# Kernel tuning notes

Hardware: AMD Instinct MI355X
Metric: run time of the kernel (lower is better)

## Reference

```python
import jax, jax.numpy as jnp
import numpy as np
import math

HIDDEN = 2048
NUM_HEADS = 32
NUM_KV_HEADS = 8
HEAD_DIM = HIDDEN // NUM_HEADS
GROUPS = NUM_HEADS // NUM_KV_HEADS
B, S = 2, 2048


def setup_inputs() -> dict:
    key = jax.random.key(0)
    ks = jax.random.split(key, 9)
    sc = 1.0 / math.sqrt(HIDDEN)
    x = jax.random.normal(ks[0], (B, S, HIDDEN), dtype=jnp.float32)
    # causal mask: 1 where attention allowed, 0 where masked
    mask = jnp.tril(jnp.ones((S, S), dtype=jnp.int32))[None, None, :, :]
    Wq = jax.random.normal(ks[1], (HIDDEN, HIDDEN), dtype=jnp.float32) * sc
    bq = jnp.zeros((HIDDEN,), dtype=jnp.float32)
    Wk = jax.random.normal(ks[2], (NUM_KV_HEADS * HEAD_DIM, HIDDEN), dtype=jnp.float32) * sc
    bk = jnp.zeros((NUM_KV_HEADS * HEAD_DIM,), dtype=jnp.float32)
    Wv = jax.random.normal(ks[3], (NUM_KV_HEADS * HEAD_DIM, HIDDEN), dtype=jnp.float32) * sc
    bv = jnp.zeros((NUM_KV_HEADS * HEAD_DIM,), dtype=jnp.float32)
    Wo = jax.random.normal(ks[4], (HIDDEN, HIDDEN), dtype=jnp.float32) * sc
    bo = jnp.zeros((HIDDEN,), dtype=jnp.float32)
    return {"x": x, "mask": mask, "Wq": Wq, "bq": bq, "Wk": Wk, "bk": bk,
            "Wv": Wv, "bv": bv, "Wo": Wo, "bo": bo}


def reference(x, mask, Wq, bq, Wk, bk, Wv, bv, Wo, bo):
    b, s, _ = x.shape
    # projections (torch Linear: y = x @ W.T + b)
    Q = (x @ Wq.T + bq).reshape(b, s, NUM_HEADS, HEAD_DIM).transpose(0, 2, 1, 3)  # b h s d
    K = (x @ Wk.T + bk).reshape(b, s, NUM_KV_HEADS, HEAD_DIM).transpose(0, 2, 1, 3)
    V = (x @ Wv.T + bv).reshape(b, s, NUM_KV_HEADS, HEAD_DIM).transpose(0, 2, 1, 3)
    # repeat_kv expansion
    K = jnp.repeat(K, GROUPS, axis=1)  # b h s d
    V = jnp.repeat(V, GROUPS, axis=1)
    scores = jnp.einsum('bhqd,bhkd->bhqk', Q, K) / math.sqrt(HEAD_DIM)
    scores = jnp.where(mask == 0, jnp.float32(-jnp.inf), scores)
    w = jax.nn.softmax(scores, axis=-1)
    # dropout is identity in eval mode
    out = jnp.einsum('bhqk,bhkd->bhqd', w, V)
    out = out.transpose(0, 2, 1, 3).reshape(b, s, HIDDEN)
    return out @ Wo.T + bo
```

## Files before the change

kernel.cpp:

```cpp
#include <hip/hip_runtime.h>
#include <hip/hip_bf16.h>
#include <stdint.h>

#define HID   2048
#define SLEN  2048
#define NB    2
#define NHEADS 32
#define NKVH   8
#define HDIM   64
#define KVW    512

typedef __bf16 bf16_t;
typedef __bf16 bf16x2 __attribute__((ext_vector_type(2)));
typedef __bf16 bf16x4 __attribute__((ext_vector_type(4)));
typedef __bf16 bf16x8 __attribute__((ext_vector_type(8)));
typedef float  f32x4  __attribute__((ext_vector_type(4)));

__device__ __forceinline__ f32x4 mfma16(bf16x8 a, bf16x8 b, f32x4 c) {
  return __builtin_amdgcn_mfma_f32_16x16x32_bf16(a, b, c, 0, 0, 0);
}

__device__ __forceinline__ void gl2lds16(const bf16_t* g, bf16_t* l) {
  __builtin_amdgcn_global_load_lds(
      (const __attribute__((address_space(1))) void*)g,
      (__attribute__((address_space(3))) void*)l,
      16, 0, 0);
}

__device__ __forceinline__ float fast_exp2(float x) {
#if __has_builtin(__builtin_amdgcn_exp2f)
  return __builtin_amdgcn_exp2f(x);
#else
  return __expf(x * 0.69314718f);
#endif
}

__device__ __forceinline__ bf16x8 ld8(const bf16_t* p) {
  return *(const bf16x8*)p;
}
__device__ __forceinline__ bf16x8 ld8(const float* p) {
  f32x4 a = *(const f32x4*)p;
  f32x4 b = *(const f32x4*)(p + 4);
  bf16x8 r;
  r[0] = (bf16_t)a[0]; r[1] = (bf16_t)a[1]; r[2] = (bf16_t)a[2]; r[3] = (bf16_t)a[3];
  r[4] = (bf16_t)b[0]; r[5] = (bf16_t)b[1]; r[6] = (bf16_t)b[2]; r[7] = (bf16_t)b[3];
  return r;
}

__device__ __forceinline__ uint32_t pack2(float a, float b) {
  bf16x2 t; t[0] = (bf16_t)a; t[1] = (bf16_t)b;
  return __builtin_bit_cast(uint32_t, t);
}

__device__ __forceinline__ void st_c(bf16_t* p, float v) { *p = (bf16_t)v; }
__device__ __forceinline__ void st_c(float*  p, float v) { *p = v; }

__global__ __launch_bounds__(256) void cvt_kernel(
    const float* __restrict__ x,  const float* __restrict__ wq,
    const float* __restrict__ wk, const float* __restrict__ wv,
    const float* __restrict__ wo,
    const float* __restrict__ bq, const float* __restrict__ bk,
    const float* __restrict__ bv,
    bf16_t* xb, bf16_t* wqb, bf16_t* wkb, bf16_t* wvb, bf16_t* wob,
    float* bcat)
{
  if (blockIdx.y >= 5) {
    const float* fs; float* fd; size_t n;
    if (blockIdx.y == 5)      { fs = bq; fd = bcat;        n = HID; }
    else if (blockIdx.y == 6) { fs = bk; fd = bcat + HID;  n = KVW; }
    else                      { fs = bv; fd = bcat + HID + KVW; n = KVW; }
    const size_t stride4 = (size_t)gridDim.x * 256 * 4;
    for (size_t i = ((size_t)blockIdx.x * 256 + threadIdx.x) * 4; i < n; i += stride4)
      *(f32x4*)(fd + i) = *(const f32x4*)(fs + i);
    return;
  }
  const float* s; bf16_t* d; size_t n;
  switch (blockIdx.y) {
    case 0:  s = x;  d = xb;  n = (size_t)NB * SLEN * HID; break;
    case 1:  s = wq; d = wqb; n = (size_t)HID * HID; break;
    case 2:  s = wk; d = wkb; n = (size_t)KVW * HID; break;
    case 3:  s = wv; d = wvb; n = (size_t)KVW * HID; break;
    default: s = wo; d = wob; n = (size_t)HID * HID; break;
  }
  const size_t stride = (size_t)gridDim.x * 256 * 8;
  for (size_t i = ((size_t)blockIdx.x * 256 + threadIdx.x) * 8; i < n; i += stride)
    *(bf16x8*)(d + i) = ld8(s + i);
}

__device__ __forceinline__ bf16x8 ldfrag(const bf16_t* __restrict__ Lh, int r, int g) {
  return *(const bf16x8*)(Lh + r * 64 + ((g ^ (r & 7)) << 3));
}

template <int N>
__device__ __forceinline__ void vm_wait() {
  if constexpr (N == 0)      asm volatile("s_waitcnt vmcnt(0)" ::: "memory");
  else if constexpr (N == 2) asm volatile("s_waitcnt vmcnt(2)" ::: "memory");
  else if constexpr (N == 3) asm volatile("s_waitcnt vmcnt(3)" ::: "memory");
  else                       asm volatile("s_waitcnt vmcnt(4)" ::: "memory");
}

template <int Q, int U>
__device__ __forceinline__ void mfma_quadU(const bf16x8 (&af)[2][2],
                                           const bf16x8 (&bfr)[U][2],
                                           f32x4 (&acc)[8][U]) {
#pragma unroll
  for (int ks = 0; ks < 2; ++ks)
#pragma unroll
    for (int i = 0; i < 2; ++i)
#pragma unroll
      for (int ni = 0; ni < U; ++ni)
        acc[2 * Q + i][ni] = mfma16(af[i][ks], bfr[ni][ks], acc[2 * Q + i][ni]);
}

__device__ __forceinline__ void phase_barrier() {
  __builtin_amdgcn_s_barrier();
  asm volatile("" ::: "memory");
}

template <int U>
__device__ __forceinline__ void gemm_core_u(
    const bf16_t* __restrict__ Ag,
    const bf16_t* __restrict__ Bg,
    bf16_t* __restrict__ lds, f32x4 (&acc)[8][U])
{
  const int tid  = threadIdx.x;
  const int lane = tid & 63;
  const int w    = tid >> 6;
  const int fr   = lane & 15;
  const int quad = lane >> 4;
  const int wr   = w >> 2;
  const int wc   = w & 3;

  bf16_t* A0 = lds;
  bf16_t* B0 = lds + 16384;
  bf16_t* A1 = B0 + U * 4096;
  bf16_t* B1 = A1 + 16384;

  const f32x4 z4 = {0.f, 0.f, 0.f, 0.f};
#pragma unroll
  for (int i = 0; i < 8; ++i)
#pragma unroll
    for (int j = 0; j < U; ++j) acc[i][j] = z4;

  auto STAGEU = [&](const bf16_t* __restrict__ Gp, bf16_t* __restrict__ Lb, int u) {
    const int r = tid >> 3;
    const int g = (tid & 7) ^ (r & 7);
    gl2lds16(Gp + (size_t)(u * 64 + r) * HID + g * 8, Lb + u * 4096 + tid * 8);
  };
  auto LDB = [&](const bf16_t* __restrict__ Bb, bf16x8 (&bfr)[U][2]) {
#pragma unroll
    for (int ni = 0; ni < U; ++ni)
#pragma unroll
      for (int ks = 0; ks < 2; ++ks)
        bfr[ni][ks] = ldfrag(Bb, wc * (16 * U) + ni * 16 + fr, ks * 4 + quad);
  };
  auto LDA = [&](const bf16_t* __restrict__ Ab, int q, bf16x8 (&af)[2][2]) {
#pragma unroll
    for (int i = 0; i < 2; ++i)
#pragma unroll
      for (int ks = 0; ks < 2; ++ks)
        af[i][ks] = ldfrag(Ab, wr * 128 + q * 32 + i * 16 + fr, ks * 4 + quad);
  };

#pragma unroll
  for (int u = 0; u < U; ++u) STAGEU(Bg, B0, u);
#pragma unroll
  for (int u = 0; u < 4; ++u) STAGEU(Ag, A0, u);
#pragma unroll
  for (int u = 0; u < U; ++u) STAGEU(Bg + 64, B1, u);
  vm_wait<U>();
  phase_barrier();

  bf16x8 bfr[U][2], af[2][2];

#pragma unroll 1
  for (int it = 0; it < 16; ++it) {
    const bool more = (it < 15);
    const size_t k1 = (size_t)(2 * it + 1) * 64;
    const size_t k2 = (size_t)(2 * it + 2) * 64;
    const size_t k3 = (size_t)(2 * it + 3) * 64;

    LDB(B0, bfr);
    LDA(A0, 0, af);
    STAGEU(Ag + k1, A1, 0); STAGEU(Ag + k1, A1, 1);
    phase_barrier();
    asm volatile("s_waitcnt lgkmcnt(0)" ::: "memory");
    __builtin_amdgcn_s_setprio(1);
    mfma_quadU<0>(af, bfr, acc);
    __builtin_amdgcn_s_setprio(0);
    phase_barrier();

    LDA(A0, 1, af);
    STAGEU(Ag + k1, A1, 2); STAGEU(Ag + k1, A1, 3);
    phase_barrier();
    asm volatile("s_waitcnt lgkmcnt(0)" ::: "memory");
    __builtin_amdgcn_s_setprio(1);
    mfma_quadU<1>(af, bfr, acc);
    __builtin_amdgcn_s_setprio(0);
    phase_barrier();

    LDA(A0, 2, af);
    if (more) {
#pragma unroll
      for (int u = 0; u < (U + 1) / 2; ++u) STAGEU(Bg + k2, B0, u);
    }
    phase_barrier();
    asm volatile("s_waitcnt lgkmcnt(0)" ::: "memory");
    __builtin_amdgcn_s_setprio(1);
    mfma_quadU<2>(af, bfr, acc);
    __builtin_amdgcn_s_setprio(0);
    phase_barrier();

    LDA(A0, 3, af);
    if (more) {
#pragma unroll
      for (int u = (U + 1) / 2; u < U; ++u) STAGEU(Bg + k2, B0, u);
    }
    phase_barrier();
    asm volatile("s_waitcnt lgkmcnt(0)" ::: "memory");
    __builtin_amdgcn_s_setprio(1);
    mfma_quadU<3>(af, bfr, acc);
    __builtin_amdgcn_s_setprio(0);
    if (more) vm_wait<U>(); else vm_wait<0>();
    phase_barrier();

    LDB(B1, bfr);
    LDA(A1, 0, af);
    if (more) { STAGEU(Ag + k2, A0, 0); STAGEU(Ag + k2, A0, 1); }
    phase_barrier();
    asm volatile("s_waitcnt lgkmcnt(0)" ::: "memory");
    __builtin_amdgcn_s_setprio(1);
    mfma_quadU<0>(af, bfr, acc);
    __builtin_amdgcn_s_setprio(0);
    phase_barrier();

    LDA(A1, 1, af);
    if (more) { STAGEU(Ag + k2, A0, 2); STAGEU(Ag + k2, A0, 3); }
    phase_barrier();
    asm volatile("s_waitcnt lgkmcnt(0)" ::: "memory");
    __builtin_amdgcn_s_setprio(1);
    mfma_quadU<1>(af, bfr, acc);
    __builtin_amdgcn_s_setprio(0);
    phase_barrier();

    LDA(A1, 2, af);
    if (more) {
#pragma unroll
      for (int u = 0; u < (U + 1) / 2; ++u) STAGEU(Bg + k3, B1, u);
    }
    phase_barrier();
    asm volatile("s_waitcnt lgkmcnt(0)" ::: "memory");
    __builtin_amdgcn_s_setprio(1);
    mfma_quadU<2>(af, bfr, acc);
    __builtin_amdgcn_s_setprio(0);
    phase_barrier();

    LDA(A1, 3, af);
    if (more) {
#pragma unroll
      for (int u = (U + 1) / 2; u < U; ++u) STAGEU(Bg + k3, B1, u);
    }
    phase_barrier();
    asm volatile("s_waitcnt lgkmcnt(0)" ::: "memory");
    __builtin_amdgcn_s_setprio(1);
    mfma_quadU<3>(af, bfr, acc);
    __builtin_amdgcn_s_setprio(0);
    if (more) vm_wait<U>();
    phase_barrier();
  }
}

__device__ __forceinline__ void grid_map16(int orig, int& cb, int& mb) {
  const int xcd = orig & 7, wp = orig >> 3;
  cb = (xcd & 1) * 8 + (wp & 7);
  mb = (xcd >> 1) * 4 + (wp >> 3);
}

__global__ __launch_bounds__(512, 2) void qkv8_kernel(
    const bf16_t* __restrict__ xb, const bf16_t* __restrict__ Wcat,
    const float* __restrict__ bcat,
    bf16_t* __restrict__ Qb, bf16_t* __restrict__ Kb, bf16_t* __restrict__ VbT)
{
  __shared__ __align__(16) bf16_t lds[57344];
  int cb, mb;
  grid_map16(blockIdx.x, cb, mb);

  f32x4 acc[8][3];
  gemm_core_u<3>(xb + (size_t)mb * 256 * HID, Wcat + (size_t)cb * 192 * HID,
                 lds, acc);

  const int tid = threadIdx.x, lane = tid & 63, w = tid >> 6;
  const int fr = lane & 15, quad = lane >> 4, wr = w >> 2, wc = w & 3;
  const int CP = 200;
  bf16_t* C = lds;
#pragma unroll
  for (int ni = 0; ni < 3; ++ni) {
    const int col = wc * 48 + ni * 16 + fr;
    const float bz = bcat[cb * 192 + col];
#pragma unroll
    for (int mi = 0; mi < 8; ++mi)
#pragma unroll
      for (int r = 0; r < 4; ++r)
        C[(wr * 128 + mi * 16 + quad * 4 + r) * CP + col] =
            (bf16_t)(acc[mi][ni][r] + bz);
  }
  asm volatile("s_waitcnt lgkmcnt(0)" ::: "memory");
  phase_barrier();

#pragma unroll
  for (int i = 0; i < 12; ++i) {
    const unsigned task = (unsigned)(i * 512 + tid);
    const unsigned row = task / 24u;
    const unsigned cg  = task - row * 24u;
    const int gcol0 = cb * 192 + (int)cg * 8;
    const int grow  = mb * 256 + (int)row;
    bf16x8 v = *(const bf16x8*)&C[row * CP + cg * 8];
    if (gcol0 < 2048)
      *(bf16x8*)&Qb[(size_t)grow * HID + gcol0] = v;
    else if (gcol0 < 2560)
      *(bf16x8*)&Kb[(size_t)grow * KVW + (gcol0 - 2048)] = v;
  }
  if (cb >= 13) {
    const int colbase = (cb == 13) ? 64 : 0;
    const int Nv = 192 - colbase;
    const int b = mb >> 3;
    const int s0 = (mb & 7) * 256;
#pragma unroll
    for (int i = 0; i < 12; ++i) {
      const int task = i * 512 + tid;
      const int vi = task >> 5, si = task & 31;
      if (vi < Nv) {
        const int col = colbase + vi;
        const int vc  = cb * 192 + col - 2560;
        bf16x8 pk;
#pragma unroll
        for (int j = 0; j < 8; ++j) pk[j] = C[(si * 8 + j) * CP + col];
        *(bf16x8*)&VbT[((size_t)(b * NKVH + (vc >> 6)) * HDIM + (vc & 63)) * SLEN
                       + s0 + si * 8] = pk;
      }
    }
  }
}

__global__ __launch_bounds__(512, 2) void oproj8_kernel(
    const bf16_t* __restrict__ A, const bf16_t* __restrict__ Wob,
    const float* __restrict__ bo, float* __restrict__ out)
{
  __shared__ __align__(16) bf16_t lds[49152];
  int cb, mb;
  grid_map16(blockIdx.x, cb, mb);

  f32x4 acc[8][2];
  gemm_core_u<2>(A + (size_t)mb * 256 * HID, Wob + (size_t)cb * 128 * HID,
                 lds, acc);

  const int tid = threadIdx.x, lane = tid & 63, w = tid >> 6;
  const int fr = lane & 15, quad = lane >> 4, wr = w >> 2, wc = w & 3;
  const int CPF = 132;
  float* Cf = (float*)lds;
#pragma unroll
  for (int s = 0; s < 2; ++s) {
    if (wr == s) {
#pragma unroll
      for (int ni = 0; ni < 2; ++ni) {
        const int col = wc * 32 + ni * 16 + fr;
        const float bz = bo[cb * 128 + col];
#pragma unroll
        for (int mi = 0; mi < 8; ++mi)
#pragma unroll
          for (int r = 0; r < 4; ++r)
            Cf[(mi * 16 + quad * 4 + r) * CPF + col] = acc[mi][ni][r] + bz;
      }
    }
    asm volatile("s_waitcnt lgkmcnt(0)" ::: "memory");
    phase_barrier();
#pragma unroll
    for (int i = 0; i < 8; ++i) {
      const int task = i * 512 + tid;
      const int row = task >> 5, cg = task & 31;
      f32x4 v = *(const f32x4*)&Cf[row * CPF + cg * 4];
      *(f32x4*)&out[(size_t)(mb * 256 + s * 128 + row) * HID + cb * 128 + cg * 4] = v;
    }
    phase_barrier();
  }
}

template <typename AT, typename CT>
__device__ __forceinline__ void gemm128_tile(
    const AT* __restrict__ Ap, int lda,
    const float* __restrict__ Wp, int ldw,
    const float* __restrict__ biasp,
    CT* __restrict__ Cp, int ldc,
    int K)
{
  __shared__ __align__(16) bf16_t Al[128 * 32];
  __shared__ __align__(16) bf16_t Bl[128 * 32];

  const int tid  = threadIdx.x;
  const int lane = tid & 63;
  const int w    = tid >> 6;
  const int fr   = lane & 15;
  const int quad = lane >> 4;
  const int wm   = (w >> 1) * 64;
  const int wn   = (w & 1) * 64;

  const f32x4 z4 = {0.f, 0.f, 0.f, 0.f};
  f32x4 acc[4][4];
  for (int i = 0; i < 4; ++i)
    for (int j = 0; j < 4; ++j) acc[i][j] = z4;

  const int c0    = w * 2;
  const int srow0 = lane >> 2;
  const int skc   = (lane & 3) * 8;

  for (int k0 = 0; k0 < K; k0 += 32) {
    bf16x8 av[2], bv[2];
    for (int t = 0; t < 2; ++t) {
      const int r = (c0 + t) * 16 + srow0;
      av[t] = ld8(Ap + (size_t)r * lda + k0 + skc);
      bv[t] = ld8(Wp + (size_t)r * ldw + k0 + skc);
    }
    for (int t = 0; t < 2; ++t) {
      const int c = c0 + t;
      *(bf16x8*)&Al[c * 512 + lane * 8] = av[t];
      *(bf16x8*)&Bl[c * 512 + lane * 8] = bv[t];
    }
    __syncthreads();
    bf16x8 af[4], bfr[4];
    for (int mi = 0; mi < 4; ++mi)
      af[mi] = *(const bf16x8*)&Al[(wm + mi * 16 + fr) * 32 + quad * 8];
    for (int ni = 0; ni < 4; ++ni)
      bfr[ni] = *(const bf16x8*)&Bl[(wn + ni * 16 + fr) * 32 + quad * 8];
    for (int mi = 0; mi < 4; ++mi)
      for (int ni = 0; ni < 4; ++ni)
        acc[mi][ni] = mfma16(af[mi], bfr[ni], acc[mi][ni]);
    __syncthreads();
  }

  for (int ni = 0; ni < 4; ++ni) {
    const int col = wn + ni * 16 + fr;
    const float bz = biasp[col];
    for (int mi = 0; mi < 4; ++mi) {
      const int r0 = wm + mi * 16 + quad * 4;
      for (int r = 0; r < 4; ++r)
        st_c(Cp + (size_t)(r0 + r) * ldc + col, acc[mi][ni][r] + bz);
    }
  }
}

__global__ __launch_bounds__(256) void qkv_kernel(
    const float* __restrict__ x,
    const float* __restrict__ Wq, const float* __restrict__ bq,
    const float* __restrict__ Wk, const float* __restrict__ bk,
    const float* __restrict__ Wv, const float* __restrict__ bv,
    bf16_t* Qb, bf16_t* Kb, bf16_t* Vb)
{
  const int nb = blockIdx.x;
  const int mb = blockIdx.y;
  const float* W; const float* bias; bf16_t* C; int ldc;
  if (nb < 16)      { W = Wq + (size_t)nb * 128 * HID;  bias = bq + nb * 128;
                      C = Qb + nb * 128; ldc = HID; }
  else if (nb < 20) { const int j = nb - 16;
                      W = Wk + (size_t)j * 128 * HID;   bias = bk + j * 128;
                      C = Kb + j * 128; ldc = KVW; }
  else              { const int j = nb - 20;
                      W = Wv + (size_t)j * 128 * HID;   bias = bv + j * 128;
                      C = Vb + j * 128; ldc = KVW; }
  gemm128_tile<float, bf16_t>(x + (size_t)mb * 128 * HID, HID, W, HID, bias,
                              C + (size_t)mb * 128 * ldc, ldc, HID);
}

__global__ __launch_bounds__(256) void oproj_kernel(
    const bf16_t* __restrict__ A, const float* __restrict__ Wo,
    const float* __restrict__ bo, float* out)
{
  const int nb = blockIdx.x, mb = blockIdx.y;
  gemm128_tile<bf16_t, float>(A + (size_t)mb * 128 * HID, HID,
                              Wo + (size_t)nb * 128 * HID, HID,
                              bo + nb * 128,
                              out + (size_t)mb * 128 * HID + nb * 128, HID, HID);
}

__global__ __launch_bounds__(256) void vtrans_kernel(
    const bf16_t* __restrict__ Vb, bf16_t* __restrict__ VbT)
{
  __shared__ bf16_t T[64][72];
  const int st = blockIdx.x, kvh = blockIdx.y, b = blockIdx.z;
  const int tid = threadIdx.x;
  {
    const int row = tid >> 2;
    const int c16 = (tid & 3) * 16;
    const bf16_t* src =
        Vb + ((size_t)b * SLEN + st * 64 + row) * KVW + kvh * HDIM + c16;
    *(bf16x8*)&T[row][c16]     = *(const bf16x8*)(src);
    *(bf16x8*)&T[row][c16 + 8] = *(const bf16x8*)(src + 8);
  }
  __syncthreads();
  {
    const int d  = tid >> 2;
    const int sc = (tid & 3) * 16;
    bf16_t tmp[16];
    for (int j = 0; j < 16; ++j) tmp[j] = T[sc + j][d];
    bf16_t* dst = VbT + ((size_t)(b * NKVH + kvh) * HDIM + d) * SLEN + st * 64 + sc;
    *(bf16x8*)dst       = *(bf16x8*)&tmp[0];
    *(bf16x8*)(dst + 8) = *(bf16x8*)&tmp[8];
  }
}

__global__ __launch_bounds__(512, 4) void attn_kernel(
    const bf16_t* Q, const bf16_t* __restrict__ Kg,
    const bf16_t* __restrict__ VT, bf16_t* O)
{
  const int bid = blockIdx.x;
  const int kvh = bid & 7;
  const int jb  = bid >> 3;
  const int b   = jb >> 5;
  const int rem = jb & 31;
  const int h   = kvh * 4 + (rem & 3);
  const int pid = rem >> 2;

  const int tid  = threadIdx.x;
  const int lane = tid & 63;
  const int w    = tid >> 6;
  const int fr   = lane & 15;
  const int quad = lane >> 4;

  __shared__ __align__(16) bf16_t lds[32768];

  const size_t qbase = (size_t)b * SLEN;
  const bf16_t* VTh = VT + (size_t)(b * NKVH + kvh) * HDIM * SLEN;

  const int sig = ((quad & 1) << 1) | ((quad >> 1) & 1);
  const int fsw = (fr >> 1) & 3;
  const bool oddq = (quad & 1);

  bf16x8 ones8;
  {
    const bf16_t o1 = (bf16_t)(fr == 0 ? 1.0f : 0.0f);
#pragma unroll
    for (int j2 = 0; j2 < 8; ++j2) ones8[j2] = o1;
  }

  auto STAGE_KV = [&](int kt, bf16_t* KL) {
    const size_t krow0 = qbase + (size_t)kt * 128;
    bf16_t* VtL = KL + 8192;
#pragma unroll
    for (int jj = 0; jj < 2; ++jj) {
      const int s  = jj * 512 + tid;
      const int ks = s >> 9, kr = (s >> 2) & 127, c8 = (s & 3) ^ ((kr >> 1) & 3);
      gl2lds16(&Kg[(krow0 + kr) * KVW + kvh * HDIM + ks * 32 + c8 * 8],
               &KL[s * 8]);
    }
#pragma unroll
    for (int jj = 0; jj < 2; ++jj) {
      const int idx = jj * 512 + tid;
      const int kb = idx >> 8, d = (idx >> 2) & 63, c8 = (idx & 3) ^ ((d >> 1) & 3);
      gl2lds16(&VTh[(size_t)d * SLEN + kt * 128 + kb * 32 + c8 * 8],
               &VtL[idx * 8]);
    }
  };

  for (int half = 0; half < 2; ++half) {
    const int qt = half ? (15 - pid) : pid;
    const int q0 = qt * 128;

    bf16x8 qf[2];
#pragma unroll
    for (int ks = 0; ks < 2; ++ks)
      qf[ks] = *(const bf16x8*)&Q[(qbase + q0 + w * 16 + fr) * HID
                                  + h * HDIM + ks * 32 + quad * 8];

    const f32x4 z4 = {0.f, 0.f, 0.f, 0.f};
    f32x4 o_acc[4];
    f32x4 o_l = z4;
#pragma unroll
    for (int di = 0; di < 4; ++di) o_acc[di] = z4;

    const int ktmax = qt;
    const int qloc  = w * 16 + fr;

    STAGE_KV(0, lds);
    asm volatile("s_waitcnt vmcnt(0)" ::: "memory");
    phase_barrier();

    int cur = 0;
    for (int kt = 0; kt <= ktmax; ++kt) {
      bf16_t* KL  = lds + cur * 16384;
      bf16_t* VtL = KL + 8192;
      if (kt < ktmax) STAGE_KV(kt + 1, lds + (cur ^ 1) * 16384);

      f32x4 s8[8];
#pragma unroll
      for (int ki = 0; ki < 8; ++ki) s8[ki] = z4;
      __builtin_amdgcn_s_setprio(1);
#pragma unroll
      for (int ks = 0; ks < 2; ++ks)
#pragma unroll
        for (int ki = 0; ki < 8; ++ki) {
          bf16x8 kf = *(const bf16x8*)&KL[ks * 4096 + (ki * 16 + fr) * 32
                                          + ((quad ^ fsw) << 3)];
          s8[ki] = mfma16(kf, qf[ks], s8[ki]);
        }
      __builtin_amdgcn_s_setprio(0);

      const float C2 = 0.18033688f;
      const bool diag = (kt == ktmax);

#pragma unroll
      for (int m = 0; m < 4; ++m) {
        float pe[8];
#pragma unroll
        for (int ki2 = 0; ki2 < 2; ++ki2) {
          const int ki = 2 * m + ki2;
#pragma unroll
          for (int r = 0; r < 4; ++r) {
            float p = fast_exp2(s8[ki][r] * C2);
            if (diag && (ki * 16 + quad * 4 + r > qloc)) p = 0.f;
            pe[ki2 * 4 + r] = p;
          }
        }
        uint32_t pw0 = pack2(pe[0], pe[1]);
        uint32_t pw1 = pack2(pe[2], pe[3]);
        uint32_t pw2 = pack2(pe[4], pe[5]);
        uint32_t pw3 = pack2(pe[6], pe[7]);
        uint32_t x0 = oddq ? pw0 : pw2;
        uint32_t x1 = oddq ? pw1 : pw3;
        uint32_t r0 = (uint32_t)__shfl_xor((int)x0, 16);
        uint32_t r1 = (uint32_t)__shfl_xor((int)x1, 16);
        union { uint32_t u[4]; bf16x8 v; } pb;
        pb.u[0] = oddq ? r0 : pw0;
        pb.u[1] = oddq ? r1 : pw1;
        pb.u[2] = oddq ? pw2 : r0;
        pb.u[3] = oddq ? pw3 : r1;

        __builtin_amdgcn_s_setprio(1);
        o_l = mfma16(pb.v, ones8, o_l);
#pragma unroll
        for (int di = 0; di < 4; ++di) {
          bf16x8 vf = *(const bf16x8*)&VtL[m * 2048 + (di * 16 + fr) * 32
                                           + ((sig ^ fsw) << 3)];
          o_acc[di] = mfma16(pb.v, vf, o_acc[di]);
        }
        __builtin_amdgcn_s_setprio(0);
      }

      asm volatile("s_waitcnt vmcnt(0)" ::: "memory");
      phase_barrier();
      cur ^= 1;
    }

    bf16_t* OB = lds;
#pragma unroll
    for (int r = 0; r < 4; ++r) {
      const float l  = __shfl(o_l[r], lane & 48);
      const float rl = 1.f / l;
      const int q = w * 16 + quad * 4 + r;
#pragma unroll
      for (int di = 0; di < 4; ++di)
        OB[q * 64 + di * 16 + fr] = (bf16_t)(o_acc[di][r] * rl);
    }
    asm volatile("s_waitcnt lgkmcnt(0)" ::: "memory");
    phase_barrier();
    {
      const int row = tid >> 2;
      const int seg = tid & 3;
      bf16x8 v0 = *(const bf16x8*)&OB[row * 64 + seg * 16];
      bf16x8 v1 = *(const bf16x8*)&OB[row * 64 + seg * 16 + 8];
      bf16_t* dst = &O[(qbase + q0 + row) * HID + h * HDIM + seg * 16];
      *(bf16x8*)dst       = v0;
      *(bf16x8*)(dst + 8) = v1;
    }
    phase_barrier();
  }
}

extern "C" void kernel_launch(void* const* d_in, const int* in_sizes, int n_in,
                              void* d_out, int out_size, void* d_ws, size_t ws_size,
                              hipStream_t stream) {
  const float* x  = (const float*)d_in[0];
  const float* Wq = (const float*)d_in[2];
  const float* bq = (const float*)d_in[3];
  const float* Wk = (const float*)d_in[4];
  const float* bk = (const float*)d_in[5];
  const float* Wv = (const float*)d_in[6];
  const float* bv = (const float*)d_in[7];
  const float* Wo = (const float*)d_in[8];
  const float* bo = (const float*)d_in[9];
  float* out = (float*)d_out;

  const size_t M = (size_t)NB * SLEN;
  dim3 blk(256, 1, 1);

  const size_t needA = (M * HID
                        + (size_t)HID * HID
                        + (size_t)KVW * HID
                        + (size_t)KVW * HID
                        + (size_t)HID * HID
                        + M * HID
                        + M * KVW
                        + M * KVW) * 2
                       + (size_t)(HID + 2 * KVW) * sizeof(float);
  if (ws_size >= needA) {
    bf16_t* xb  = (bf16_t*)d_ws;
    bf16_t* Wqb = xb  + M * HID;
    bf16_t* Wkb = Wqb + (size_t)HID * HID;
    bf16_t* Wvb = Wkb + (size_t)KVW * HID;
    bf16_t* Wob = Wvb + (size_t)KVW * HID;
    bf16_t* Qb  = Wob + (size_t)HID * HID;
    bf16_t* Kb  = Qb  + M * HID;
    bf16_t* VbT = Kb  + M * KVW;
    float*  bcat = (float*)(VbT + M * KVW);

    cvt_kernel<<<dim3(1024, 8, 1), blk, 0, stream>>>(
        x, Wq, Wk, Wv, Wo, bq, bk, bv, xb, Wqb, Wkb, Wvb, Wob, bcat);
    qkv8_kernel<<<dim3(256, 1, 1), dim3(512, 1, 1), 0, stream>>>(
        xb, Wqb, bcat, Qb, Kb, VbT);
    attn_kernel<<<dim3(512, 1, 1), dim3(512, 1, 1), 0, stream>>>(Qb, Kb, VbT, Qb);
    oproj8_kernel<<<dim3(256, 1, 1), dim3(512, 1, 1), 0, stream>>>(
        Qb, Wob, bo, out);
  } else {
    bf16_t* Qb  = (bf16_t*)d_ws;
    bf16_t* Kb  = Qb + M * HID;
    bf16_t* Vb  = Kb + M * KVW;
    bf16_t* VbT = Vb + M * KVW;

    qkv_kernel<<<dim3(24, 32, 1), blk, 0, stream>>>(x, Wq, bq, Wk, bk, Wv, bv, Qb, Kb, Vb);
    vtrans_kernel<<<dim3(32, 8, 2), blk, 0, stream>>>(Vb, VbT);
    attn_kernel<<<dim3(512, 1, 1), dim3(512, 1, 1), 0, stream>>>(Qb, Kb, VbT, Qb);
    oproj_kernel<<<dim3(16, 32, 1), blk, 0, stream>>>(Qb, Wo, bo, out);
  }
}
```

Before: 285.8 us.

## Halve GEMM phases per k-tile and swizzle QKV epilogue LDS staging

The GEMM main loop now loads A fragments for half the warp tile (64 rows) at once and issues twice as many MFMAs per phase. That cuts the number of barrier-separated phases per k-tile from four to two, and global-to-LDS staging is regrouped into whole-tile batches. Separately, the QKV epilogue writes C into LDS with an XOR swizzle on 8-element column groups to reduce bank conflicts in both the row-wise and the transposed V reads. The trade-off is more live A-fragment registers and coarser interleaving of loads with math.

New measurement: 273.6 us. -4.3%, faster.

```diff
diff --git a/kernel.cpp b/kernel.cpp
--- a/kernel.cpp
+++ b/kernel.cpp
@@ -99,17 +99,20 @@
   else                       asm volatile("s_waitcnt vmcnt(4)" ::: "memory");
 }
 
-template <int Q, int U>
-__device__ __forceinline__ void mfma_quadU(const bf16x8 (&af)[2][2],
+template <int H, int U>
+__device__ __forceinline__ void mfma_halfU(const bf16x8 (&af2)[2][2][2],
                                            const bf16x8 (&bfr)[U][2],
                                            f32x4 (&acc)[8][U]) {
 #pragma unroll
-  for (int ks = 0; ks < 2; ++ks)
-#pragma unroll
-    for (int i = 0; i < 2; ++i)
-#pragma unroll
-      for (int ni = 0; ni < U; ++ni)
-        acc[2 * Q + i][ni] = mfma16(af[i][ks], bfr[ni][ks], acc[2 * Q + i][ni]);
+  for (int q = 0; q < 2; ++q)
+#pragma unroll
+    for (int ks = 0; ks < 2; ++ks)
+#pragma unroll
+      for (int i = 0; i < 2; ++i)
+#pragma unroll
+        for (int ni = 0; ni < U; ++ni)
+          acc[4 * H + 2 * q + i][ni] =
+              mfma16(af2[q][i][ks], bfr[ni][ks], acc[4 * H + 2 * q + i][ni]);
 }
 
 __device__ __forceinline__ void phase_barrier() {
@@ -154,12 +157,15 @@
       for (int ks = 0; ks < 2; ++ks)
         bfr[ni][ks] = ldfrag(Bb, wc * (16 * U) + ni * 16 + fr, ks * 4 + quad);
   };
-  auto LDA = [&](const bf16_t* __restrict__ Ab, int q, bf16x8 (&af)[2][2]) {
-#pragma unroll
-    for (int i = 0; i < 2; ++i)
-#pragma unroll
-      for (int ks = 0; ks < 2; ++ks)
-        af[i][ks] = ldfrag(Ab, wr * 128 + q * 32 + i * 16 + fr, ks * 4 + quad);
+  auto LDAH = [&](const bf16_t* __restrict__ Ab, int h, bf16x8 (&af2)[2][2][2]) {
+#pragma unroll
+    for (int q = 0; q < 2; ++q)
+#pragma unroll
+      for (int i = 0; i < 2; ++i)
+#pragma unroll
+        for (int ks = 0; ks < 2; ++ks)
+          af2[q][i][ks] =
+              ldfrag(Ab, wr * 128 + h * 64 + q * 32 + i * 16 + fr, ks * 4 + quad);
   };
 
 #pragma unroll
@@ -171,7 +177,7 @@
   vm_wait<U>();
   phase_barrier();
 
-  bf16x8 bfr[U][2], af[2][2];
+  bf16x8 bfr[U][2], af2[2][2][2];
 
 #pragma unroll 1
   for (int it = 0; it < 16; ++it) {
@@ -181,89 +187,51 @@
     const size_t k3 = (size_t)(2 * it + 3) * 64;
 
     LDB(B0, bfr);
-    LDA(A0, 0, af);
-    STAGEU(Ag + k1, A1, 0); STAGEU(Ag + k1, A1, 1);
+    LDAH(A0, 0, af2);
+#pragma unroll
+    for (int u = 0; u < 4; ++u) STAGEU(Ag + k1, A1, u);
     phase_barrier();
     asm volatile("s_waitcnt lgkmcnt(0)" ::: "memory");
     __builtin_amdgcn_s_setprio(1);
-    mfma_quadU<0>(af, bfr, acc);
+    mfma_halfU<0>(af2, bfr, acc);
     __builtin_amdgcn_s_setprio(0);
     phase_barrier();
 
-    LDA(A0, 1, af);
-    STAGEU(Ag + k1, A1, 2); STAGEU(Ag + k1, A1, 3);
+    LDAH(A0, 1, af2);
+    if (more) {
+#pragma unroll
+      for (int u = 0; u < U; ++u) STAGEU(Bg + k2, B0, u);
+    }
     phase_barrier();
     asm volatile("s_waitcnt lgkmcnt(0)" ::: "memory");
     __builtin_amdgcn_s_setprio(1);
-    mfma_quadU<1>(af, bfr, acc);
+    mfma_halfU<1>(af2, bfr, acc);
     __builtin_amdgcn_s_setprio(0);
-    phase_barrier();
-
-    LDA(A0, 2, af);
+    if (more) vm_wait<U>(); else vm_wait<0>();
+    phase_barrier();
+
+    LDB(B1, bfr);
+    LDAH(A1, 0, af2);
     if (more) {
 #pragma unroll
-      for (int u = 0; u < (U + 1) / 2; ++u) STAGEU(Bg + k2, B0, u);
+      for (int u = 0; u < 4; ++u) STAGEU(Ag + k2, A0, u);
     }
     phase_barrier();
     asm volatile("s_waitcnt lgkmcnt(0)" ::: "memory");
     __builtin_amdgcn_s_setprio(1);
-    mfma_quadU<2>(af, bfr, acc);
+    mfma_halfU<0>(af2, bfr, acc);
     __builtin_amdgcn_s_setprio(0);
     phase_barrier();
 
-    LDA(A0, 3, af);
+    LDAH(A1, 1, af2);
     if (more) {
 #pragma unroll
-      for (int u = (U + 1) / 2; u < U; ++u) STAGEU(Bg + k2, B0, u);
+      for (int u = 0; u < U; ++u) STAGEU(Bg + k3, B1, u);
     }
     phase_barrier();
     asm volatile("s_waitcnt lgkmcnt(0)" ::: "memory");
     __builtin_amdgcn_s_setprio(1);
-    mfma_quadU<3>(af, bfr, acc);
-    __builtin_amdgcn_s_setprio(0);
-    if (more) vm_wait<U>(); else vm_wait<0>();
-    phase_barrier();
-
-    LDB(B1, bfr);
-    LDA(A1, 0, af);
-    if (more) { STAGEU(Ag + k2, A0, 0); STAGEU(Ag + k2, A0, 1); }
-    phase_barrier();
-    asm volatile("s_waitcnt lgkmcnt(0)" ::: "memory");
-    __builtin_amdgcn_s_setprio(1);
-    mfma_quadU<0>(af, bfr, acc);
-    __builtin_amdgcn_s_setprio(0);
-    phase_barrier();
-
-    LDA(A1, 1, af);
-    if (more) { STAGEU(Ag + k2, A0, 2); STAGEU(Ag + k2, A0, 3); }
-    phase_barrier();
-    asm volatile("s_waitcnt lgkmcnt(0)" ::: "memory");
-    __builtin_amdgcn_s_setprio(1);
-    mfma_quadU<1>(af, bfr, acc);
-    __builtin_amdgcn_s_setprio(0);
-    phase_barrier();
-
-    LDA(A1, 2, af);
-    if (more) {
-#pragma unroll
-      for (int u = 0; u < (U + 1) / 2; ++u) STAGEU(Bg + k3, B1, u);
-    }
-    phase_barrier();
-    asm volatile("s_waitcnt lgkmcnt(0)" ::: "memory");
-    __builtin_amdgcn_s_setprio(1);
-    mfma_quadU<2>(af, bfr, acc);
-    __builtin_amdgcn_s_setprio(0);
-    phase_barrier();
-
-    LDA(A1, 3, af);
-    if (more) {
-#pragma unroll
-      for (int u = (U + 1) / 2; u < U; ++u) STAGEU(Bg + k3, B1, u);
-    }
-    phase_barrier();
-    asm volatile("s_waitcnt lgkmcnt(0)" ::: "memory");
-    __builtin_amdgcn_s_setprio(1);
-    mfma_quadU<3>(af, bfr, acc);
+    mfma_halfU<1>(af2, bfr, acc);
     __builtin_amdgcn_s_setprio(0);
     if (more) vm_wait<U>();
     phase_barrier();
@@ -276,6 +244,12 @@
   mb = (xcd >> 1) * 4 + (wp >> 3);
 }
 
+__device__ __forceinline__ int cswz(int row, int col, int CP) {
+  const int cg = col >> 3;
+  const int g  = (cg & ~7) | ((cg ^ (row >> 3)) & 7);
+  return row * CP + (g << 3) + (col & 7);
+}
+
 __global__ __launch_bounds__(512, 2) void qkv8_kernel(
     const bf16_t* __restrict__ xb, const bf16_t* __restrict__ Wcat,
     const float* __restrict__ bcat,
@@ -301,7 +275,7 @@
     for (int mi = 0; mi < 8; ++mi)
 #pragma unroll
       for (int r = 0; r < 4; ++r)
-        C[(wr * 128 + mi * 16 + quad * 4 + r) * CP + col] =
+        C[cswz(wr * 128 + mi * 16 + quad * 4 + r, col, CP)] =
             (bf16_t)(acc[mi][ni][r] + bz);
   }
   asm volatile("s_waitcnt lgkmcnt(0)" ::: "memory");
@@ -314,7 +288,8 @@
     const unsigned cg  = task - row * 24u;
     const int gcol0 = cb * 192 + (int)cg * 8;
     const int grow  = mb * 256 + (int)row;
-    bf16x8 v = *(const bf16x8*)&C[row * CP + cg * 8];
+    const int g = ((int)cg & ~7) | (((int)cg ^ ((int)row >> 3)) & 7);
+    bf16x8 v = *(const bf16x8*)&C[(int)row * CP + (g << 3)];
     if (gcol0 < 2048)
       *(bf16x8*)&Qb[(size_t)grow * HID + gcol0] = v;
     else if (gcol0 < 2560)
@@ -334,7 +309,7 @@
         const int vc  = cb * 192 + col - 2560;
         bf16x8 pk;
 #pragma unroll
-        for (int j = 0; j < 8; ++j) pk[j] = C[(si * 8 + j) * CP + col];
+        for (int j = 0; j < 8; ++j) pk[j] = C[cswz(si * 8 + j, col, CP)];
         *(bf16x8*)&VbT[((size_t)(b * NKVH + (vc >> 6)) * HDIM + (vc & 63)) * SLEN
                        + s0 + si * 8] = pk;
       }
```
